# Optimization experiments

Hardware: AMD Instinct MI355X
Metric: run time of the kernel (lower is better)

Reference implementation:

```python
import jax, jax.numpy as jnp
import numpy as np

NUM_EXPERTS = 64
TOP_K = 2
CAPACITY_FACTOR = 1.25
D_MODEL = 2048
BATCH, SEQ = 4, 4096


def setup_inputs() -> dict:
    key = jax.random.key(0)
    kx, kw = jax.random.split(key)
    x = jax.random.normal(kx, (BATCH, SEQ, D_MODEL), dtype=jnp.float32)
    # router weight: Linear(input_dim, num_experts, bias=False), init std=0.001
    W = jax.random.normal(kw, (NUM_EXPERTS, D_MODEL), dtype=jnp.float32) * 0.001
    return {"x": x, "W": W}


def reference(x, W):
    B, S, D = x.shape
    N = B * S  # combined batch of tokens
    E = NUM_EXPERTS
    k = TOP_K
    capacity = int(CAPACITY_FACTOR * N * k / E)  # static Python int

    x_flat = x.reshape(N, D)
    router_logits = jnp.einsum('nd,ed->ne', x_flat, W)  # [N, E]
    routing_weights = jax.nn.softmax(router_logits, axis=-1)

    top_k_weights, top_k_indices = jax.lax.top_k(routing_weights, k)  # [N, k]
    top_k_weights = top_k_weights / (top_k_weights.sum(-1, keepdims=True) + 1e-8)

    expert_counts = jnp.zeros((E,), dtype=jnp.float32)
    dispatch_mask = jnp.zeros((N, E), dtype=jnp.float32)
    token_ids = jnp.arange(N)

    # Sequential over k (fixed, small): within a k-step the capacity check uses
    # counts from previous steps only, matching the torch scatter semantics.
    for k_idx in range(k):
        expert_idx = top_k_indices[:, k_idx]            # [N]
        under_cap = expert_counts[expert_idx] < capacity  # [N] bool
        expert_counts = expert_counts + jax.ops.segment_sum(
            under_cap.astype(jnp.float32), expert_idx, num_segments=E)
        # top-k experts are distinct per token, so add == set on zero-init slots
        dispatch_mask = dispatch_mask.at[token_ids, expert_idx].add(
            jnp.where(under_cap, top_k_weights[:, k_idx], 0.0))

    # Tokens that got dropped everywhere go to the least-loaded expert with w=1
    unrouted = dispatch_mask.sum(-1) == 0                     # [N]
    least_loaded = jnp.argmax(capacity - expert_counts)       # scalar
    dispatch_mask = jnp.where(
        unrouted[:, None] & (jnp.arange(E)[None, :] == least_loaded),
        1.0, dispatch_mask)

    normalized_dispatch_mask = dispatch_mask / (dispatch_mask.sum(-1, keepdims=True) + 1e-8)

    router_z_loss = jnp.mean(jnp.square(router_logits))
    counts = normalized_dispatch_mask.sum(0)                  # [E]
    target_count = float(N * k / E)
    load_balance_loss = jnp.mean(jnp.square(counts / float(N) - target_count / float(N)))
    router_loss = 0.001 * jax.lax.stop_gradient(router_z_loss) \
                + 0.001 * jax.lax.stop_gradient(load_balance_loss)

    return (jax.lax.stop_gradient(routing_weights), normalized_dispatch_mask, router_loss)
```

## Files before the change

kernel.cpp:

```cpp
#include <hip/hip_runtime.h>
#include <math.h>

#define N_TOK 16384
#define D_MODEL 2048
#define N_EXP 64
#define CAPACITY 640
#define NREP 8
#define NS 64

typedef __attribute__((ext_vector_type(8))) _Float16 h8;
typedef __attribute__((ext_vector_type(4))) float f4;

__global__ __launch_bounds__(256) void k0_cvtw(const float* __restrict__ W,
                                               _Float16* __restrict__ WTH,
                                               _Float16* __restrict__ WTL) {
  const int t = threadIdx.x;
  const int lane = t & 63;
  const int c = blockIdx.x * 4 + (t >> 6);
  const int e = (c & 3) * 16 + (lane & 15);
  const int k = (c >> 2) * 32 + (lane >> 4) * 8;
  const float* src = W + (size_t)e * D_MODEL + k;
  const float4 a = *(const float4*)src;
  const float4 b = *(const float4*)(src + 4);
  const float f[8] = {a.x, a.y, a.z, a.w, b.x, b.y, b.z, b.w};
  h8 hh, ll;
#pragma unroll
  for (int j = 0; j < 8; j++) {
    const float s = f[j] * 1024.f;
    const _Float16 h = (_Float16)s;
    hh[j] = h;
    ll[j] = (_Float16)((s - (float)h) * 1024.f);
  }
  *(h8*)(WTH + c * 512 + lane * 8) = hh;
  *(h8*)(WTL + c * 512 + lane * 8) = ll;
}

__global__ __launch_bounds__(128, 4) void k12_gemm_softmax(
    const float* __restrict__ x, const _Float16* __restrict__ WTH,
    const _Float16* __restrict__ WTL, float* __restrict__ rw_out,
    int2* __restrict__ top12, float2* __restrict__ wts,
    int* __restrict__ histR, float* __restrict__ zR) {
  __shared__ float slog[16][65];
  __shared__ float zred[2];

  const int t = threadIdx.x;
  const int lane = t & 63;
  const int wn = t >> 6;
  const int m0 = blockIdx.x * 16;
  const int rep = blockIdx.x & (NREP - 1);

  const int frow = lane & 15;
  const int fk = (lane >> 4) * 8;

  const float* xg = x + (size_t)(m0 + frow) * D_MODEL + fk;
  const _Float16* wth = WTH + (wn * 2) * 512 + lane * 8;
  const _Float16* wtl = WTL + (wn * 2) * 512 + lane * 8;

  float4 xr[4][2];
  h8 wh_[2][2], wl_[2][2];
  f4 acc1[2], acc2[2];
#pragma unroll
  for (int i = 0; i < 2; i++) {
    acc1[i] = (f4)(0.f);
    acc2[i] = (f4)(0.f);
  }

#define LX(sl, s)                          \
  {                                        \
    const float* p_ = xg + (s) * 32;       \
    xr[sl][0] = *(const float4*)p_;        \
    xr[sl][1] = *(const float4*)(p_ + 4);  \
  }
#define LW(sl, s)                              \
  {                                            \
    const _Float16* ph_ = wth + (s) * 2048;    \
    const _Float16* pl_ = wtl + (s) * 2048;    \
    wh_[sl][0] = *(const h8*)ph_;              \
    wh_[sl][1] = *(const h8*)(ph_ + 512);      \
    wl_[sl][0] = *(const h8*)pl_;              \
    wl_[sl][1] = *(const h8*)(pl_ + 512);      \
  }
#define STEP(xs, ws, s)                                                     \
  {                                                                         \
    h8 ah, al;                                                              \
    {                                                                       \
      const float xf[8] = {xr[xs][0].x, xr[xs][0].y, xr[xs][0].z,           \
                           xr[xs][0].w, xr[xs][1].x, xr[xs][1].y,           \
                           xr[xs][1].z, xr[xs][1].w};                       \
      _Pragma("unroll") for (int j = 0; j < 8; j++) {                       \
        const _Float16 a_ = (_Float16)xf[j];                                \
        ah[j] = a_;                                                         \
        al[j] = (_Float16)((xf[j] - (float)a_) * 1024.f);                   \
      }                                                                     \
    }                                                                       \
    _Pragma("unroll") for (int nt = 0; nt < 2; nt++) {                      \
      acc1[nt] = __builtin_amdgcn_mfma_f32_16x16x32_f16(ah, wh_[ws][nt],    \
                                                        acc1[nt], 0, 0, 0); \
      acc2[nt] = __builtin_amdgcn_mfma_f32_16x16x32_f16(al, wh_[ws][nt],    \
                                                        acc2[nt], 0, 0, 0); \
      acc2[nt] = __builtin_amdgcn_mfma_f32_16x16x32_f16(ah, wl_[ws][nt],    \
                                                        acc2[nt], 0, 0, 0); \
    }                                                                       \
    if ((s) + 2 < NS) LW(ws, (s) + 2);                                      \
    if ((s) + 4 < NS) LX(xs, (s) + 4);                                      \
  }

  LX(0, 0);
  LX(1, 1);
  LX(2, 2);
  LX(3, 3);
  LW(0, 0);
  LW(1, 1);

  for (int g = 0; g < NS; g += 4) {
    STEP(0, 0, g);
    STEP(1, 1, g + 1);
    STEP(2, 0, g + 2);
    STEP(3, 1, g + 3);
  }

  const int cg = lane >> 4, ci = lane & 15;
#pragma unroll
  for (int nt = 0; nt < 2; nt++)
#pragma unroll
    for (int r = 0; r < 4; r++) {
      const float v =
          (acc1[nt][r] + acc2[nt][r] * 0.0009765625f) * 0.0009765625f;
      slog[cg * 4 + r][wn * 32 + nt * 16 + ci] = v;
    }
  __syncthreads();

  float z_acc = 0.f;
  for (int tt = 0; tt < 8; tt++) {
    const int tloc = wn * 8 + tt;
    const int n = m0 + tloc;
    const float v = slog[tloc][lane];
    z_acc += v * v;
    float mx = v;
#pragma unroll
    for (int off = 32; off; off >>= 1) mx = fmaxf(mx, __shfl_xor(mx, off));
    const float p = __expf(v - mx);
    float ssum = p;
#pragma unroll
    for (int off = 32; off; off >>= 1) ssum += __shfl_xor(ssum, off);
    const float rw = p / ssum;
    rw_out[(size_t)n * N_EXP + lane] = rw;

    const unsigned long long b1 = __ballot(v == mx);
    const int i1 = __builtin_ctzll(b1);
    float v2 = (lane == i1) ? -INFINITY : v;
#pragma unroll
    for (int off = 32; off; off >>= 1) v2 = fmaxf(v2, __shfl_xor(v2, off));
    const unsigned long long b2 = __ballot(v == v2) & ~(1ull << i1);
    const int i2 = __builtin_ctzll(b2);
    const float rw1 = __shfl(rw, i1);
    const float rw2 = __shfl(rw, i2);
    if (lane == 0) {
      const float denom = rw1 + rw2 + 1e-8f;
      top12[n] = make_int2(i1, i2);
      wts[n] = make_float2(rw1 / denom, rw2 / denom);
      atomicAdd(&histR[(rep * N_EXP + i1) * 16], 1);
    }
  }
#pragma unroll
  for (int off = 32; off; off >>= 1) z_acc += __shfl_xor(z_acc, off);
  if (lane == 0) zred[wn] = z_acc;
  __syncthreads();
  if (t == 0) atomicAdd(&zR[rep * 16], zred[0] + zred[1]);
}

__global__ __launch_bounds__(256) void k3_dispatch(
    const int2* __restrict__ top12, const float2* __restrict__ wts,
    const int* __restrict__ histR, float* __restrict__ mask_out,
    float* __restrict__ cntR) {
  const int lane = threadIdx.x & 63;
  const int wid = threadIdx.x >> 6;
  const int n = blockIdx.x * 4 + wid;
  const int rep = blockIdx.x & (NREP - 1);

  const int2 ij = top12[n];
  const float2 w = wts[n];
  int h = 0;
#pragma unroll
  for (int r = 0; r < NREP; r++) h += histR[(r * N_EXP + ij.y) * 16];
  const bool allowed = h < CAPACITY;
  const float ssum = w.x + (allowed ? w.y : 0.f);
  const float inv = 1.f / (ssum + 1e-8f);
  float val = 0.f;
  if (lane == ij.x) val = w.x * inv;
  else if (allowed && lane == ij.y) val = w.y * inv;
  mask_out[(size_t)n * N_EXP + lane] = val;
  if (val != 0.f) atomicAdd(&cntR[(rep * N_EXP + lane) * 16], val);
}

__global__ void k4_loss(const float* __restrict__ cntR,
                        const float* __restrict__ zR,
                        float* __restrict__ loss_out) {
  const int lane = threadIdx.x;
  float c = 0.f;
#pragma unroll
  for (int r = 0; r < NREP; r++) c += cntR[(r * N_EXP + lane) * 16];
  const float d = (c - 512.0f) * (1.0f / 16384.0f);
  float v = d * d;
#pragma unroll
  for (int off = 32; off; off >>= 1) v += __shfl_xor(v, off);
  if (lane == 0) {
    float z = 0.f;
#pragma unroll
    for (int r = 0; r < NREP; r++) z += zR[r * 16];
    const float lb = v * (1.0f / 64.0f);
    loss_out[0] = 0.001f * (z * (1.0f / (16384.0f * 64.0f))) + 0.001f * lb;
  }
}

extern "C" void kernel_launch(void* const* d_in, const int* in_sizes, int n_in,
                              void* d_out, int out_size, void* d_ws,
                              size_t ws_size, hipStream_t stream) {
  const float* x = (const float*)d_in[0];
  const float* W = (const float*)d_in[1];
  float* out = (float*)d_out;
  float* rw_out = out;
  float* mask_out = out + (size_t)N_TOK * N_EXP;
  float* loss_out = out + 2 * (size_t)N_TOK * N_EXP;

  char* ws = (char*)d_ws;
  int* histR = (int*)ws;
  float* cntR = (float*)(ws + 32768);
  float* zR = (float*)(ws + 65536);
  int2* top12 = (int2*)(ws + 131072);
  float2* wts = (float2*)(ws + 262144);
  _Float16* WTH = (_Float16*)(ws + 393216);
  _Float16* WTL = (_Float16*)(ws + 655360);

  hipMemsetAsync(histR, 0, 65536 + 512, stream);
  k0_cvtw<<<64, 256, 0, stream>>>(W, WTH, WTL);
  k12_gemm_softmax<<<1024, 128, 0, stream>>>(x, WTH, WTL, rw_out, top12, wts,
                                             histR, zR);
  k3_dispatch<<<N_TOK / 4, 256, 0, stream>>>(top12, wts, histR, mask_out,
                                             cntR);
  k4_loss<<<1, 64, 0, stream>>>(cntR, zR, loss_out);
}
```

Measured before the change: 229.7 us.

## Split GEMM expert tiles across four waves and deepen x prefetch pipeline

The router GEMM block grows from 128 to 256 threads, so each of four waves computes one 16-expert tile instead of two waves each handling two. Each wave now keeps eight k-steps of x loads in flight rather than four, and sched_barriers pin the order of loads and MFMAs. The goal is more memory-level parallelism and latency hiding on the x stream. The cost is that every wave redundantly loads and converts the same x rows, doubling x fetch and split-conversion work per block and adding register pressure.

```diff
diff --git a/kernel.cpp b/kernel.cpp
--- a/kernel.cpp
+++ b/kernel.cpp
@@ -35,13 +35,13 @@
   *(h8*)(WTL + c * 512 + lane * 8) = ll;
 }
 
-__global__ __launch_bounds__(128, 4) void k12_gemm_softmax(
+__global__ __launch_bounds__(256, 4) void k12_gemm_softmax(
     const float* __restrict__ x, const _Float16* __restrict__ WTH,
     const _Float16* __restrict__ WTL, float* __restrict__ rw_out,
     int2* __restrict__ top12, float2* __restrict__ wts,
     int* __restrict__ histR, float* __restrict__ zR) {
   __shared__ float slog[16][65];
-  __shared__ float zred[2];
+  __shared__ float zred[4];
 
   const int t = threadIdx.x;
   const int lane = t & 63;
@@ -53,86 +53,96 @@
   const int fk = (lane >> 4) * 8;
 
   const float* xg = x + (size_t)(m0 + frow) * D_MODEL + fk;
-  const _Float16* wth = WTH + (wn * 2) * 512 + lane * 8;
-  const _Float16* wtl = WTL + (wn * 2) * 512 + lane * 8;
-
-  float4 xr[4][2];
-  h8 wh_[2][2], wl_[2][2];
-  f4 acc1[2], acc2[2];
-#pragma unroll
-  for (int i = 0; i < 2; i++) {
-    acc1[i] = (f4)(0.f);
-    acc2[i] = (f4)(0.f);
-  }
-
-#define LX(sl, s)                          \
-  {                                        \
-    const float* p_ = xg + (s) * 32;       \
-    xr[sl][0] = *(const float4*)p_;        \
-    xr[sl][1] = *(const float4*)(p_ + 4);  \
-  }
-#define LW(sl, s)                              \
-  {                                            \
-    const _Float16* ph_ = wth + (s) * 2048;    \
-    const _Float16* pl_ = wtl + (s) * 2048;    \
-    wh_[sl][0] = *(const h8*)ph_;              \
-    wh_[sl][1] = *(const h8*)(ph_ + 512);      \
-    wl_[sl][0] = *(const h8*)pl_;              \
-    wl_[sl][1] = *(const h8*)(pl_ + 512);      \
-  }
-#define STEP(xs, ws, s)                                                     \
-  {                                                                         \
-    h8 ah, al;                                                              \
-    {                                                                       \
-      const float xf[8] = {xr[xs][0].x, xr[xs][0].y, xr[xs][0].z,           \
-                           xr[xs][0].w, xr[xs][1].x, xr[xs][1].y,           \
-                           xr[xs][1].z, xr[xs][1].w};                       \
-      _Pragma("unroll") for (int j = 0; j < 8; j++) {                       \
-        const _Float16 a_ = (_Float16)xf[j];                                \
-        ah[j] = a_;                                                         \
-        al[j] = (_Float16)((xf[j] - (float)a_) * 1024.f);                   \
-      }                                                                     \
-    }                                                                       \
-    _Pragma("unroll") for (int nt = 0; nt < 2; nt++) {                      \
-      acc1[nt] = __builtin_amdgcn_mfma_f32_16x16x32_f16(ah, wh_[ws][nt],    \
-                                                        acc1[nt], 0, 0, 0); \
-      acc2[nt] = __builtin_amdgcn_mfma_f32_16x16x32_f16(al, wh_[ws][nt],    \
-                                                        acc2[nt], 0, 0, 0); \
-      acc2[nt] = __builtin_amdgcn_mfma_f32_16x16x32_f16(ah, wl_[ws][nt],    \
-                                                        acc2[nt], 0, 0, 0); \
-    }                                                                       \
-    if ((s) + 2 < NS) LW(ws, (s) + 2);                                      \
-    if ((s) + 4 < NS) LX(xs, (s) + 4);                                      \
-  }
-
-  LX(0, 0);
-  LX(1, 1);
-  LX(2, 2);
-  LX(3, 3);
-  LW(0, 0);
-  LW(1, 1);
-
-  for (int g = 0; g < NS; g += 4) {
-    STEP(0, 0, g);
-    STEP(1, 1, g + 1);
-    STEP(2, 0, g + 2);
-    STEP(3, 1, g + 3);
-  }
+  const _Float16* wth = WTH + wn * 512 + lane * 8;
+  const _Float16* wtl = WTL + wn * 512 + lane * 8;
+
+  float4 xr[8][2];
+  h8 wh_[2], wl_[2];
+  f4 acc1 = (f4)(0.f), acc2 = (f4)(0.f);
+
+#define LX(sl, s)                         \
+  {                                       \
+    const float* p_ = xg + (s) * 32;      \
+    xr[sl][0] = *(const float4*)p_;       \
+    xr[sl][1] = *(const float4*)(p_ + 4); \
+  }
+#define LW(sl, s)                               \
+  {                                             \
+    wh_[sl] = *(const h8*)(wth + (s) * 2048);   \
+    wl_[sl] = *(const h8*)(wtl + (s) * 2048);   \
+  }
+#define CVT_MFMA(xs, ws)                                                  \
+  {                                                                       \
+    h8 ah, al;                                                            \
+    const float xf[8] = {xr[xs][0].x, xr[xs][0].y, xr[xs][0].z,           \
+                         xr[xs][0].w, xr[xs][1].x, xr[xs][1].y,           \
+                         xr[xs][1].z, xr[xs][1].w};                       \
+    _Pragma("unroll") for (int j = 0; j < 8; j++) {                       \
+      const _Float16 a_ = (_Float16)xf[j];                                \
+      ah[j] = a_;                                                         \
+      al[j] = (_Float16)((xf[j] - (float)a_) * 1024.f);                   \
+    }                                                                     \
+    acc1 = __builtin_amdgcn_mfma_f32_16x16x32_f16(ah, wh_[ws], acc1, 0, 0, \
+                                                  0);                      \
+    acc2 = __builtin_amdgcn_mfma_f32_16x16x32_f16(al, wh_[ws], acc2, 0, 0, \
+                                                  0);                      \
+    acc2 = __builtin_amdgcn_mfma_f32_16x16x32_f16(ah, wl_[ws], acc2, 0, 0, \
+                                                  0);                      \
+  }
+#define STEP_FULL(xs, ws, s)             \
+  {                                      \
+    CVT_MFMA(xs, ws);                    \
+    LW(ws, (s) + 2);                     \
+    LX(xs, (s) + 8);                     \
+    __builtin_amdgcn_sched_barrier(0);   \
+  }
+#define STEP_W(xs, ws, s)                \
+  {                                      \
+    CVT_MFMA(xs, ws);                    \
+    LW(ws, (s) + 2);                     \
+    __builtin_amdgcn_sched_barrier(0);   \
+  }
+#define STEP_N(xs, ws)                   \
+  {                                      \
+    CVT_MFMA(xs, ws);                    \
+    __builtin_amdgcn_sched_barrier(0);   \
+  }
+
+  LX(0, 0); LX(1, 1); LX(2, 2); LX(3, 3);
+  LX(4, 4); LX(5, 5); LX(6, 6); LX(7, 7);
+  LW(0, 0); LW(1, 1);
+  __builtin_amdgcn_sched_barrier(0);
+
+  for (int g = 0; g < 56; g += 8) {
+    STEP_FULL(0, 0, g);
+    STEP_FULL(1, 1, g + 1);
+    STEP_FULL(2, 0, g + 2);
+    STEP_FULL(3, 1, g + 3);
+    STEP_FULL(4, 0, g + 4);
+    STEP_FULL(5, 1, g + 5);
+    STEP_FULL(6, 0, g + 6);
+    STEP_FULL(7, 1, g + 7);
+  }
+  STEP_W(0, 0, 56);
+  STEP_W(1, 1, 57);
+  STEP_W(2, 0, 58);
+  STEP_W(3, 1, 59);
+  STEP_W(4, 0, 60);
+  STEP_W(5, 1, 61);
+  STEP_N(6, 0);
+  STEP_N(7, 1);
 
   const int cg = lane >> 4, ci = lane & 15;
 #pragma unroll
-  for (int nt = 0; nt < 2; nt++)
-#pragma unroll
-    for (int r = 0; r < 4; r++) {
-      const float v =
-          (acc1[nt][r] + acc2[nt][r] * 0.0009765625f) * 0.0009765625f;
-      slog[cg * 4 + r][wn * 32 + nt * 16 + ci] = v;
-    }
+  for (int r = 0; r < 4; r++) {
+    const float v = (acc1[r] + acc2[r] * 0.0009765625f) * 0.0009765625f;
+    slog[cg * 4 + r][wn * 16 + ci] = v;
+  }
   __syncthreads();
 
   float z_acc = 0.f;
-  for (int tt = 0; tt < 8; tt++) {
-    const int tloc = wn * 8 + tt;
+  for (int tt = 0; tt < 4; tt++) {
+    const int tloc = wn * 4 + tt;
     const int n = m0 + tloc;
     const float v = slog[tloc][lane];
     z_acc += v * v;
@@ -166,7 +176,7 @@
   for (int off = 32; off; off >>= 1) z_acc += __shfl_xor(z_acc, off);
   if (lane == 0) zred[wn] = z_acc;
   __syncthreads();
-  if (t == 0) atomicAdd(&zR[rep * 16], zred[0] + zred[1]);
+  if (t == 0) atomicAdd(&zR[rep * 16], zred[0] + zred[1] + zred[2] + zred[3]);
 }
 
 __global__ __launch_bounds__(256) void k3_dispatch(
@@ -234,7 +244,7 @@
 
   hipMemsetAsync(histR, 0, 65536 + 512, stream);
   k0_cvtw<<<64, 256, 0, stream>>>(W, WTH, WTL);
-  k12_gemm_softmax<<<1024, 128, 0, stream>>>(x, WTH, WTL, rw_out, top12, wts,
+  k12_gemm_softmax<<<1024, 256, 0, stream>>>(x, WTH, WTL, rw_out, top12, wts,
                                              histR, zR);
   k3_dispatch<<<N_TOK / 4, 256, 0, stream>>>(top12, wts, histR, mask_out,
                                              cntR);
```

Result: slower. 323.6 us (+40.9%).
